# Optimization experiments

Measured on AMD Instinct MI355X. Metric: run time of the kernel, lower is better.

Reference implementation:

```python
import jax, jax.numpy as jnp
import numpy as np

B, L1, L2 = 4, 1024, 512
D_PG, D_EX = 2304, 1024
H, HKV, DH = 8, 4, 256
SCALE = 256.0 ** -0.5


def _rope(x, cos, sin):
    # x: [B, L, h, DH]; cos/sin: [B, L, 1, DH//2]
    x = x.astype(jnp.float32)
    x1, x2 = jnp.split(x, 2, axis=-1)
    return jnp.concatenate([x1 * cos - x2 * sin, x2 * cos + x1 * sin], axis=-1)


def setup_inputs() -> dict:
    key = jax.random.key(0)
    ks = jax.random.split(key, 16)
    s = 0.02
    return {
        "pg_embeds": jax.random.normal(ks[0], (B, L1, D_PG), jnp.float32),
        "ex_embeds": jax.random.normal(ks[1], (B, L2, D_EX), jnp.float32),
        "cos": jax.random.normal(ks[2], (B, L1 + L2, 1, DH // 2), jnp.float32),
        "sin": jax.random.normal(ks[3], (B, L1 + L2, 1, DH // 2), jnp.float32),
        "attention_mask": jnp.zeros((B, L1 + L2, L1 + L2), jnp.float32),
        "Wq0": jax.random.normal(ks[4], (H * DH, D_PG), jnp.float32) * s,
        "Wk0": jax.random.normal(ks[5], (HKV * DH, D_PG), jnp.float32) * s,
        "Wv0": jax.random.normal(ks[6], (HKV * DH, D_PG), jnp.float32) * s,
        "Wo0": jax.random.normal(ks[7], (D_PG, H * DH), jnp.float32) * s,
        "Wq1": jax.random.normal(ks[8], (H * DH, D_EX), jnp.float32) * s,
        "Wk1": jax.random.normal(ks[9], (HKV * DH, D_EX), jnp.float32) * s,
        "Wv1": jax.random.normal(ks[10], (HKV * DH, D_EX), jnp.float32) * s,
        "Wo1": jax.random.normal(ks[11], (D_EX, H * DH), jnp.float32) * s,
    }


def reference(pg_embeds, ex_embeds, cos, sin, attention_mask,
              Wq0, Wk0, Wv0, Wo0, Wq1, Wk1, Wv1, Wo1):
    b, l1 = pg_embeds.shape[0], pg_embeds.shape[1]
    l2 = ex_embeds.shape[1]
    # per-stream QKV projections, then concat along sequence
    q = jnp.concatenate([
        (pg_embeds @ Wq0.T).reshape(b, l1, H, DH),
        (ex_embeds @ Wq1.T).reshape(b, l2, H, DH)], axis=1)
    k = jnp.concatenate([
        (pg_embeds @ Wk0.T).reshape(b, l1, HKV, DH),
        (ex_embeds @ Wk1.T).reshape(b, l2, HKV, DH)], axis=1)
    v = jnp.concatenate([
        (pg_embeds @ Wv0.T).reshape(b, l1, HKV, DH),
        (ex_embeds @ Wv1.T).reshape(b, l2, HKV, DH)], axis=1)
    q = _rope(q, cos, sin)  # fp32
    k = _rope(k, cos, sin)
    # GQA: repeat KV heads to match query heads
    rep = H // HKV
    k = jnp.repeat(k, rep, axis=2)
    v = jnp.repeat(jnp.repeat(v, rep, axis=2).astype(jnp.float32), 1, axis=0)
    # scores: [B, H, L, L]
    scores = jnp.einsum('bqhd,bkhd->bhqk', q, k) * SCALE
    scores = scores + attention_mask[:, None, :, :]
    p = jax.nn.softmax(scores, axis=-1)
    att = jnp.einsum('bhqk,bkhd->bqhd', p, v).reshape(b, l1 + l2, H * DH)
    out0 = att[:, :l1] @ Wo0.T
    out1 = att[:, l1:] @ Wo1.T
    return (out0, out1)
```

## Files before the change

kernel.cpp:

```cpp
#include <hip/hip_runtime.h>
#include <stdint.h>
#include <stddef.h>


typedef _Float16 f16;
typedef _Float16 f16x8 __attribute__((ext_vector_type(8)));
typedef _Float16 f16x4 __attribute__((ext_vector_type(4)));
typedef float    f32x4 __attribute__((ext_vector_type(4)));

__device__ __forceinline__ void async_ld16(const void* g, void* l) {
  __builtin_amdgcn_global_load_lds((const __attribute__((address_space(1))) void*)g,
                                   (__attribute__((address_space(3))) void*)l,
                                   16, 0, 0);
}

template <typename Epi>
__device__ __forceinline__ void gemm_pipe(f16* lds,
    const f16* __restrict__ A, int lda,
    const f16* __restrict__ B, int ldb,
    int K, Epi&& epi)
{
  const int t    = threadIdx.x;
  const int w    = t >> 6;
  const int lane = t & 63;
  const int q4   = lane >> 4;
  const int l16  = lane & 15;
  const int wm   = w >> 1;
  const int wn   = w & 1;

  const int srow = w * 16 + (lane >> 2);
  const int scol = (lane & 3) * 8;
  const f16* aP = A + (size_t)srow * lda + scol;
  const f16* bP = B + (size_t)srow * ldb + scol;
  const size_t a128 = (size_t)128 * lda;
  const int wl = w * 512;

  const int arow = (wm * 64 + l16) * 32 + q4 * 8;
  const int brow = (wn * 64 + l16) * 32 + q4 * 8;

  f32x4 acc[4][4];
  const f32x4 vz = {0.f, 0.f, 0.f, 0.f};
#pragma unroll
  for (int i = 0; i < 4; ++i)
#pragma unroll
    for (int j = 0; j < 4; ++j) acc[i][j] = vz;

  async_ld16(aP,             lds + wl);
  async_ld16(aP + a128,      lds + 4096 + wl);
  async_ld16(bP,             lds + 32768 + wl);
  asm volatile("" ::: "memory");
  async_ld16(aP + 32,        lds + 8192 + wl);
  async_ld16(aP + a128 + 32, lds + 8192 + 4096 + wl);
  async_ld16(bP + 32,        lds + 32768 + 4096 + wl);
  asm volatile("s_waitcnt vmcnt(3)" ::: "memory");
  asm volatile("s_barrier" ::: "memory");

  const int NT = K >> 6;
  int cb = 0;
  for (int tk = 0; tk < NT; ++tk) {
    f16* aT = lds + cb * 16384;
    f16* bT = lds + 32768 + cb * 8192;
    f16* aD = lds + (cb ^ 1) * 16384;
    f16* bD = lds + 32768 + (cb ^ 1) * 8192;
    const int kn = (tk + 1) << 6;
    const bool st = tk < NT - 1;
#pragma unroll
    for (int s = 0; s < 2; ++s) {
      const f16* aS = aT + s * 8192;
      const f16* bS = bT + s * 4096;
      f16x8 af[4], bf[4];
#pragma unroll
      for (int i = 0; i < 4; ++i) {
        af[i] = *(const f16x8*)(aS + arow + i * 512);
        bf[i] = *(const f16x8*)(bS + brow + i * 512);
      }
      if (st) {
        if (s == 0) {
          async_ld16(aP + kn,        aD + wl);
          async_ld16(aP + a128 + kn, aD + 4096 + wl);
          async_ld16(bP + kn,        bD + wl);
        } else {
          async_ld16(aP + kn + 32,        aD + 8192 + wl);
          async_ld16(aP + a128 + kn + 32, aD + 8192 + 4096 + wl);
          async_ld16(bP + kn + 32,        bD + 4096 + wl);
        }
        asm volatile("s_waitcnt vmcnt(3)" ::: "memory");
      } else if (s == 0) {
        asm volatile("s_waitcnt vmcnt(0)" ::: "memory");
      }
      asm volatile("s_barrier" ::: "memory");
      __builtin_amdgcn_s_setprio(1);
#pragma unroll
      for (int mi = 0; mi < 4; ++mi)
#pragma unroll
        for (int ni = 0; ni < 4; ++ni)
          acc[mi][ni] = __builtin_amdgcn_mfma_f32_16x16x32_f16(af[mi], bf[ni], acc[mi][ni], 0, 0, 0);
      __builtin_amdgcn_s_setprio(0);
      asm volatile("s_barrier" ::: "memory");
    }
    cb ^= 1;
  }

#pragma unroll
  for (int mi = 0; mi < 4; ++mi)
#pragma unroll
    for (int ni = 0; ni < 4; ++ni)
#pragma unroll
      for (int r = 0; r < 4; ++r)
        epi(wm * 64 + mi * 16 + q4 * 4 + r, wn * 64 + ni * 16 + l16, acc[mi][ni][r]);
}

__global__ __launch_bounds__(512, 2) void k_qkv3(
    const f16* __restrict__ xpg, const f16* __restrict__ xex,
    const f16* __restrict__ W0,  const f16* __restrict__ W1,
    f16* __restrict__ q, f16* __restrict__ k, f16* __restrict__ v)
{
  __shared__ alignas(16) f16 lds[49152];
  const int idx = blockIdx.x;
  int by, bx, K; const f16 *A, *B;
  const bool s0 = idx < 512;
  if (s0) { by = idx >> 5; bx = idx & 31; K = 2304;
            A = xpg + (size_t)by * 256 * 2304; B = W0 + (size_t)bx * 128 * 2304; }
  else    { int j = idx - 512; by = j >> 5; bx = j & 31; K = 1024;
            A = xex + (size_t)by * 256 * 1024; B = W1 + (size_t)bx * 128 * 1024; }

  f16* D; int ldd, coff;
  if (bx < 16)      { D = q; ldd = 2048; coff = 0; }
  else if (bx < 24) { D = k; ldd = 1024; coff = 2048; }
  else              { D = v; ldd = 1024; coff = 3072; }
  const int colb = bx * 128 - coff;
  const int rowb = s0 ? ((by >> 2) * 1536 + (by & 3) * 256)
                      : ((by >> 1) * 1536 + 1024 + (by & 1) * 256);

  gemm_pipe(lds, A, K, B, K, K, [&](int r, int c, float fv) {
    D[(size_t)(rowb + r) * ldd + colb + c] = (f16)fv;
  });
}

__global__ __launch_bounds__(256) void k_post(
    f16* __restrict__ q, f16* __restrict__ k,
    const float* __restrict__ cs, const float* __restrict__ sn,
    const float* __restrict__ msk, f16* __restrict__ mkh,
    const f16* __restrict__ v, f16* __restrict__ vt)
{
  const int blk = blockIdx.x;
  if (blk < 6144) {
    __shared__ f16 tile[32][33];
    const int b = blk / 1536, r0 = blk % 1536;
    const int d0 = (r0 & 31) * 32, l0 = (r0 >> 5) * 32;
    const int t = threadIdx.x;
    const int tr = t >> 5, tc = t & 31;
#pragma unroll
    for (int i = 0; i < 4; ++i)
      tile[tr + i * 8][tc] = v[((size_t)b * 1536 + l0 + tr + i * 8) * 1024 + d0 + tc];
    __syncthreads();
#pragma unroll
    for (int i = 0; i < 4; ++i) {
      int d = d0 + tr + i * 8;
      vt[(((size_t)b * 4 + (d >> 8)) * 256 + (d & 255)) * 1536 + l0 + tc] = tile[tc][tr + i * 8];
    }
  } else if (blk < 15360) {
    const size_t gid = ((size_t)(blk - 6144) * 256 + threadIdx.x) * 4;
    float4 m4 = *(const float4*)(msk + gid);
    f16x4 o = {(f16)m4.x, (f16)m4.y, (f16)m4.z, (f16)m4.w};
    *(f16x4*)(mkh + gid) = o;
  } else {
    const size_t tid8 = ((size_t)(blk - 15360) * 256 + threadIdx.x) * 8;
    f16* base; size_t row; int col;
    if (tid8 < 12582912ull) { base = q + tid8; row = tid8 >> 11; col = (int)(tid8 & 2047); }
    else { size_t f = tid8 - 12582912ull; base = k + f; row = f >> 10; col = (int)(f & 1023); }
    const int j0 = (col & 255) >> 1;
    f16x8 x = *(const f16x8*)base;
    float4 c4 = *(const float4*)(cs + row * 128 + j0);
    float4 s4 = *(const float4*)(sn + row * 128 + j0);
    f16x8 o;
    const float cc[4] = {c4.x, c4.y, c4.z, c4.w};
    const float ss[4] = {s4.x, s4.y, s4.z, s4.w};
#pragma unroll
    for (int p = 0; p < 4; ++p) {
      float x1 = (float)x[2 * p], x2 = (float)x[2 * p + 1];
      o[2 * p]     = (f16)(x1 * cc[p] - x2 * ss[p]);
      o[2 * p + 1] = (f16)(x2 * cc[p] + x1 * ss[p]);
    }
    *(f16x8*)base = o;
  }
}

__global__ __launch_bounds__(512, 2) void k_attn2(
    const f16* __restrict__ qb, const f16* __restrict__ kb,
    const f16* __restrict__ mask, f16* __restrict__ Sdst,
    const f16* __restrict__ Psrc, const f16* __restrict__ vt,
    f16* __restrict__ att0, f16* __restrict__ att1,
    const f16* __restrict__ wo0, const f16* __restrict__ wo1,
    float* __restrict__ out0, float* __restrict__ out1,
    int b_sc, int b_pv, int b_op, int npv, int nop)
{
  __shared__ alignas(16) f16 lds[49152];
  const int idx = blockIdx.x;
  if (idx < nop) {
    int by, bx, ldc, rowb; const f16 *A, *B; float* C;
    if (idx < 72) { by = idx / 18; bx = idx % 18;
                    A = att0 + (size_t)(b_op * 4 + by) * 256 * 2048;
                    B = wo0 + (size_t)bx * 128 * 2048;
                    C = out0; ldc = 2304; rowb = b_op * 1024 + by * 256; }
    else          { int j = idx - 72; by = j >> 3; bx = j & 7;
                    A = att1 + (size_t)(b_op * 2 + by) * 256 * 2048;
                    B = wo1 + (size_t)bx * 128 * 2048;
                    C = out1; ldc = 1024; rowb = b_op * 512 + by * 256; }
    const int colb = bx * 128;
    gemm_pipe(lds, A, 2048, B, 2048, 2048, [&](int r, int c, float fv) {
      C[(size_t)(rowb + r) * ldc + colb + c] = fv;
    });
  } else if (idx < nop + npv) {
    const int j = idx - nop;
    const int h = j / 12, rem = j % 12, by = rem >> 1, bx = rem & 1;
    const f16* A = Psrc + (size_t)h * 1536 * 1536 + (size_t)by * 256 * 1536;
    const f16* B = vt + (size_t)(b_pv * 4 + (h >> 1)) * 256 * 1536 + (size_t)bx * 128 * 1536;
    f16* dst = (by < 4)
      ? att0 + (size_t)(b_pv * 1024 + by * 256) * 2048 + h * 256 + bx * 128
      : att1 + (size_t)(b_pv * 512 + (by - 4) * 256) * 2048 + h * 256 + bx * 128;
    gemm_pipe(lds, A, 1536, B, 1536, 1536, [&](int r, int c, float fv) {
      dst[(size_t)r * 2048 + c] = (f16)fv;
    });
  } else {
    const int j = idx - nop - npv;
    const int h = j / 72, rem = j % 72, by = rem / 12, bx = rem % 12;
    const f16* A = qb + (size_t)b_sc * 1536 * 2048 + h * 256 + (size_t)by * 256 * 2048;
    const f16* B = kb + (size_t)b_sc * 1536 * 1024 + (h >> 1) * 256 + (size_t)bx * 128 * 1024;
    f16* Sz = Sdst + (size_t)h * 1536 * 1536 + (size_t)by * 256 * 1536 + bx * 128;
    const f16* mb = mask + (size_t)b_sc * 1536 * 1536 + (size_t)by * 256 * 1536 + bx * 128;
    gemm_pipe(lds, A, 2048, B, 1024, 256, [&](int r, int c, float fv) {
      size_t i = (size_t)r * 1536 + c;
      Sz[i] = (f16)(fv * 0.0625f + (float)mb[i]);
    });
  }
}

__global__ __launch_bounds__(256) void k_softmax(f16* __restrict__ S)
{
  const int row = blockIdx.x * 4 + (threadIdx.x >> 6);
  const int lane = threadIdx.x & 63;
  f16* p = S + (size_t)row * 1536 + lane * 8;
  f16x8 v0 = *(const f16x8*)p;
  f16x8 v1 = *(const f16x8*)(p + 512);
  f16x8 v2 = *(const f16x8*)(p + 1024);
  float x[24];
#pragma unroll
  for (int i = 0; i < 8; ++i) {
    x[i] = (float)v0[i]; x[8 + i] = (float)v1[i]; x[16 + i] = (float)v2[i];
  }
  float mx = x[0];
#pragma unroll
  for (int i = 1; i < 24; ++i) mx = fmaxf(mx, x[i]);
#pragma unroll
  for (int o = 32; o > 0; o >>= 1) mx = fmaxf(mx, __shfl_xor(mx, o, 64));
  float s = 0.f;
#pragma unroll
  for (int i = 0; i < 24; ++i) { x[i] = __expf(x[i] - mx); s += x[i]; }
#pragma unroll
  for (int o = 32; o > 0; o >>= 1) s += __shfl_xor(s, o, 64);
  const float inv = 1.f / s;
  f16x8 o0, o1, o2;
#pragma unroll
  for (int i = 0; i < 8; ++i) {
    o0[i] = (f16)(x[i] * inv); o1[i] = (f16)(x[8 + i] * inv); o2[i] = (f16)(x[16 + i] * inv);
  }
  *(f16x8*)p = o0; *(f16x8*)(p + 512) = o1; *(f16x8*)(p + 1024) = o2;
}

__global__ __launch_bounds__(256) void k_cast_all(
    const float* __restrict__ s0, const float* __restrict__ s1,
    const float* __restrict__ s2, const float* __restrict__ s3,
    const float* __restrict__ s4, const float* __restrict__ s5,
    f16* __restrict__ ws)
{
  const size_t gid = ((size_t)blockIdx.x * 256 + threadIdx.x) * 4;
  const float* s; size_t off, dst;
  if      (gid < 9437184ull)  { s = s0; off = gid;               dst = 0ull        + off; }
  else if (gid < 11534336ull) { s = s1; off = gid - 9437184ull;  dst = 9437184ull  + off; }
  else if (gid < 13893632ull) { s = s2; off = gid - 11534336ull; dst = 18612224ull + off; }
  else if (gid < 18612224ull) { s = s3; off = gid - 13893632ull; dst = 20971520ull + off; }
  else if (gid < 19660800ull) { s = s4; off = gid - 18612224ull; dst = 28835840ull + off; }
  else                        { s = s5; off = gid - 19660800ull; dst = 29884416ull + off; }
  float4 v = *(const float4*)(s + off);
  f16x4 o = {(f16)v.x, (f16)v.y, (f16)v.z, (f16)v.w};
  *(f16x4*)(ws + dst) = o;
}

__global__ __launch_bounds__(256) void k_cast_wr(
    const float* __restrict__ wq0, const float* __restrict__ wk0,
    const float* __restrict__ wq1, const float* __restrict__ wk1,
    f16* __restrict__ W0c, f16* __restrict__ W1c)
{
  const int idx = blockIdx.x;
  const float* src; f16* dstm; int K, r, drow;
  if      (idx < 2048) { src = wq0; dstm = W0c; K = 2304; r = idx;        drow = idx; }
  else if (idx < 3072) { src = wk0; dstm = W0c; K = 2304; r = idx - 2048; drow = idx; }
  else if (idx < 5120) { src = wq1; dstm = W1c; K = 1024; r = idx - 3072; drow = idx - 3072; }
  else                 { src = wk1; dstm = W1c; K = 1024; r = idx - 5120; drow = idx - 3072; }
  const int w = r & 255;
  const int srow = (r & ~255) + (w >> 1) + ((w & 1) << 7);
  const float* sp = src + (size_t)srow * K;
  f16* dp = dstm + (size_t)drow * K;
  for (int c = threadIdx.x * 4; c < K; c += 1024) {
    float4 v = *(const float4*)(sp + c);
    f16x4 o = {(f16)v.x, (f16)v.y, (f16)v.z, (f16)v.w};
    *(f16x4*)(dp + c) = o;
  }
}

extern "C" void kernel_launch(void* const* d_in, const int* in_sizes, int n_in,
                              void* d_out, int out_size, void* d_ws, size_t ws_size,
                              hipStream_t stream)
{
  (void)in_sizes; (void)n_in; (void)out_size; (void)ws_size;
  const float* pg  = (const float*)d_in[0];
  const float* ex  = (const float*)d_in[1];
  const float* cs  = (const float*)d_in[2];
  const float* sn  = (const float*)d_in[3];
  const float* msk = (const float*)d_in[4];

  char* ws = (char*)d_ws;
  f16* xpg  = (f16*)(ws + 0);
  f16* xex  = (f16*)(ws + 18874368);
  f16* W0c  = (f16*)(ws + 23068672);
  f16* wo0c = (f16*)(ws + 41943040);
  f16* W1c  = (f16*)(ws + 51380224);
  f16* wo1c = (f16*)(ws + 59768832);
  f16* qb   = (f16*)(ws + 63963136);
  f16* kb   = (f16*)(ws + 89128960);
  f16* vb   = (f16*)(ws + 101711872);
  f16* vt   = (f16*)(ws + 114294784);
  f16* att0 = (f16*)(ws + 126877696);
  f16* att1 = (f16*)(ws + 143654912);
  f16* S0   = (f16*)(ws + 152043520);
  f16* S1   = (f16*)(ws + 189792256);
  f16* mkh  = W0c;
  float* out0 = (float*)d_out;
  float* out1 = out0 + 9437184;

  k_cast_all<<<21248, 256, 0, stream>>>(
      pg, ex, (const float*)d_in[7], (const float*)d_in[8],
      (const float*)d_in[11], (const float*)d_in[12], (f16*)ws);
  k_cast_wr<<<6144, 256, 0, stream>>>(
      (const float*)d_in[5], (const float*)d_in[6],
      (const float*)d_in[9], (const float*)d_in[10], W0c, W1c);

  k_qkv3<<<768, 512, 0, stream>>>(xpg, xex, W0c, W1c, qb, kb, vb);

  k_post<<<24576, 256, 0, stream>>>(qb, kb, cs, sn, msk, mkh, vb, vt);

  k_attn2<<<576, 512, 0, stream>>>(qb, kb, mkh, S0, S0, vt, att0, att1, wo0c, wo1c, out0, out1, 0, 0, 0, 0, 0);
  k_softmax<<<3072, 256, 0, stream>>>(S0);
  k_attn2<<<672, 512, 0, stream>>>(qb, kb, mkh, S1, S0, vt, att0, att1, wo0c, wo1c, out0, out1, 1, 0, 0, 96, 0);
  k_softmax<<<3072, 256, 0, stream>>>(S1);
  k_attn2<<<760, 512, 0, stream>>>(qb, kb, mkh, S0, S1, vt, att0, att1, wo0c, wo1c, out0, out1, 2, 1, 0, 96, 88);
  k_softmax<<<3072, 256, 0, stream>>>(S0);
  k_attn2<<<760, 512, 0, stream>>>(qb, kb, mkh, S1, S0, vt, att0, att1, wo0c, wo1c, out0, out1, 3, 2, 1, 96, 88);
  k_softmax<<<3072, 256, 0, stream>>>(S1);

  k_attn2<<<184, 512, 0, stream>>>(qb, kb, mkh, S0, S1, vt, att0, att1, wo0c, wo1c, out0, out1, 0, 3, 2, 96, 88);
  k_attn2<<<88, 512, 0, stream>>>(qb, kb, mkh, S0, S1, vt, att0, att1, wo0c, wo1c, out0, out1, 0, 0, 3, 0, 88);
}
```

Baseline: 649.2 us.

## Triple-buffer GEMM pipeline with 32-K stages, XCD block swizzle, raise occupancy bound

Replaces the double-buffered 64-wide K loop, which had two sub-steps, with a three-stage ring of 32-wide K tiles. Each stage is prefetched two iterations ahead, and there is one barrier pair per step. LDS per block shrinks from 96KB to 72KB. Blocks are remapped with an 8-way interleave so that consecutive logical tiles land on the same XCD and share L2. Launch bounds are raised to 4 blocks per CU. Asking for that occupancy may force register caps that spill the 64-float accumulator, and the LDS footprint may still only allow 2 blocks per CU.

```diff
diff --git a/kernel.cpp b/kernel.cpp
--- a/kernel.cpp
+++ b/kernel.cpp
@@ -12,6 +12,10 @@
   __builtin_amdgcn_global_load_lds((const __attribute__((address_space(1))) void*)g,
                                    (__attribute__((address_space(3))) void*)l,
                                    16, 0, 0);
+}
+
+__device__ __forceinline__ int xswz(int bid, int n) {
+  return (bid & 7) * (n >> 3) + (bid >> 3);
 }
 
 template <typename Epi>
@@ -45,61 +49,46 @@
 #pragma unroll
     for (int j = 0; j < 4; ++j) acc[i][j] = vz;
 
-  async_ld16(aP,             lds + wl);
-  async_ld16(aP + a128,      lds + 4096 + wl);
-  async_ld16(bP,             lds + 32768 + wl);
+#define STAGE3(kt, bi)                                            \
+  { const int kk_ = (kt) << 5; f16* d_ = lds + (bi) * 12288;      \
+    async_ld16(aP + kk_,        d_ + wl);                         \
+    async_ld16(aP + a128 + kk_, d_ + 4096 + wl);                  \
+    async_ld16(bP + kk_,        d_ + 8192 + wl); }
+
+  STAGE3(0, 0);
   asm volatile("" ::: "memory");
-  async_ld16(aP + 32,        lds + 8192 + wl);
-  async_ld16(aP + a128 + 32, lds + 8192 + 4096 + wl);
-  async_ld16(bP + 32,        lds + 32768 + 4096 + wl);
-  asm volatile("s_waitcnt vmcnt(3)" ::: "memory");
-  asm volatile("s_barrier" ::: "memory");
-
-  const int NT = K >> 6;
-  int cb = 0;
+  STAGE3(1, 1);
+
+  const int NT = K >> 5;
+  int cur = 0;
   for (int tk = 0; tk < NT; ++tk) {
-    f16* aT = lds + cb * 16384;
-    f16* bT = lds + 32768 + cb * 8192;
-    f16* aD = lds + (cb ^ 1) * 16384;
-    f16* bD = lds + 32768 + (cb ^ 1) * 8192;
-    const int kn = (tk + 1) << 6;
-    const bool st = tk < NT - 1;
-#pragma unroll
-    for (int s = 0; s < 2; ++s) {
-      const f16* aS = aT + s * 8192;
-      const f16* bS = bT + s * 4096;
-      f16x8 af[4], bf[4];
-#pragma unroll
-      for (int i = 0; i < 4; ++i) {
-        af[i] = *(const f16x8*)(aS + arow + i * 512);
-        bf[i] = *(const f16x8*)(bS + brow + i * 512);
-      }
-      if (st) {
-        if (s == 0) {
-          async_ld16(aP + kn,        aD + wl);
-          async_ld16(aP + a128 + kn, aD + 4096 + wl);
-          async_ld16(bP + kn,        bD + wl);
-        } else {
-          async_ld16(aP + kn + 32,        aD + 8192 + wl);
-          async_ld16(aP + a128 + kn + 32, aD + 8192 + 4096 + wl);
-          async_ld16(bP + kn + 32,        bD + 4096 + wl);
-        }
-        asm volatile("s_waitcnt vmcnt(3)" ::: "memory");
-      } else if (s == 0) {
-        asm volatile("s_waitcnt vmcnt(0)" ::: "memory");
-      }
-      asm volatile("s_barrier" ::: "memory");
-      __builtin_amdgcn_s_setprio(1);
-#pragma unroll
-      for (int mi = 0; mi < 4; ++mi)
-#pragma unroll
-        for (int ni = 0; ni < 4; ++ni)
-          acc[mi][ni] = __builtin_amdgcn_mfma_f32_16x16x32_f16(af[mi], bf[ni], acc[mi][ni], 0, 0, 0);
-      __builtin_amdgcn_s_setprio(0);
-      asm volatile("s_barrier" ::: "memory");
+    if (tk == NT - 1) asm volatile("s_waitcnt vmcnt(0)" ::: "memory");
+    else              asm volatile("s_waitcnt vmcnt(3)" ::: "memory");
+    asm volatile("s_barrier" ::: "memory");
+
+    const f16* aS = lds + cur * 12288;
+    const f16* bS = aS + 8192;
+    f16x8 af[4], bf[4];
+#pragma unroll
+    for (int i = 0; i < 4; ++i) {
+      af[i] = *(const f16x8*)(aS + arow + i * 512);
+      bf[i] = *(const f16x8*)(bS + brow + i * 512);
     }
-    cb ^= 1;
-  }
+    if (tk + 2 < NT) {
+      int nb = cur + 2; if (nb >= 3) nb -= 3;
+      STAGE3(tk + 2, nb);
+    }
+    __builtin_amdgcn_s_setprio(1);
+#pragma unroll
+    for (int mi = 0; mi < 4; ++mi)
+#pragma unroll
+      for (int ni = 0; ni < 4; ++ni)
+        acc[mi][ni] = __builtin_amdgcn_mfma_f32_16x16x32_f16(af[mi], bf[ni], acc[mi][ni], 0, 0, 0);
+    __builtin_amdgcn_s_setprio(0);
+    asm volatile("s_barrier" ::: "memory");
+    ++cur; if (cur == 3) cur = 0;
+  }
+#undef STAGE3
 
 #pragma unroll
   for (int mi = 0; mi < 4; ++mi)
@@ -110,13 +99,13 @@
         epi(wm * 64 + mi * 16 + q4 * 4 + r, wn * 64 + ni * 16 + l16, acc[mi][ni][r]);
 }
 
-__global__ __launch_bounds__(512, 2) void k_qkv3(
+__global__ __launch_bounds__(512, 4) void k_qkv4(
     const f16* __restrict__ xpg, const f16* __restrict__ xex,
     const f16* __restrict__ W0,  const f16* __restrict__ W1,
     f16* __restrict__ q, f16* __restrict__ k, f16* __restrict__ v)
 {
-  __shared__ alignas(16) f16 lds[49152];
-  const int idx = blockIdx.x;
+  __shared__ alignas(16) f16 lds[36864];
+  const int idx = xswz(blockIdx.x, 768);
   int by, bx, K; const f16 *A, *B;
   const bool s0 = idx < 512;
   if (s0) { by = idx >> 5; bx = idx & 31; K = 2304;
@@ -186,7 +175,7 @@
   }
 }
 
-__global__ __launch_bounds__(512, 2) void k_attn2(
+__global__ __launch_bounds__(512, 4) void k_attn3(
     const f16* __restrict__ qb, const f16* __restrict__ kb,
     const f16* __restrict__ mask, f16* __restrict__ Sdst,
     const f16* __restrict__ Psrc, const f16* __restrict__ vt,
@@ -195,8 +184,8 @@
     float* __restrict__ out0, float* __restrict__ out1,
     int b_sc, int b_pv, int b_op, int npv, int nop)
 {
-  __shared__ alignas(16) f16 lds[49152];
-  const int idx = blockIdx.x;
+  __shared__ alignas(16) f16 lds[36864];
+  const int idx = xswz(blockIdx.x, (int)gridDim.x);
   if (idx < nop) {
     int by, bx, ldc, rowb; const f16 *A, *B; float* C;
     if (idx < 72) { by = idx / 18; bx = idx % 18;
@@ -346,19 +335,19 @@
       (const float*)d_in[5], (const float*)d_in[6],
       (const float*)d_in[9], (const float*)d_in[10], W0c, W1c);
 
-  k_qkv3<<<768, 512, 0, stream>>>(xpg, xex, W0c, W1c, qb, kb, vb);
+  k_qkv4<<<768, 512, 0, stream>>>(xpg, xex, W0c, W1c, qb, kb, vb);
 
   k_post<<<24576, 256, 0, stream>>>(qb, kb, cs, sn, msk, mkh, vb, vt);
 
-  k_attn2<<<576, 512, 0, stream>>>(qb, kb, mkh, S0, S0, vt, att0, att1, wo0c, wo1c, out0, out1, 0, 0, 0, 0, 0);
+  k_attn3<<<576, 512, 0, stream>>>(qb, kb, mkh, S0, S0, vt, att0, att1, wo0c, wo1c, out0, out1, 0, 0, 0, 0, 0);
   k_softmax<<<3072, 256, 0, stream>>>(S0);
-  k_attn2<<<672, 512, 0, stream>>>(qb, kb, mkh, S1, S0, vt, att0, att1, wo0c, wo1c, out0, out1, 1, 0, 0, 96, 0);
+  k_attn3<<<672, 512, 0, stream>>>(qb, kb, mkh, S1, S0, vt, att0, att1, wo0c, wo1c, out0, out1, 1, 0, 0, 96, 0);
   k_softmax<<<3072, 256, 0, stream>>>(S1);
-  k_attn2<<<760, 512, 0, stream>>>(qb, kb, mkh, S0, S1, vt, att0, att1, wo0c, wo1c, out0, out1, 2, 1, 0, 96, 88);
+  k_attn3<<<760, 512, 0, stream>>>(qb, kb, mkh, S0, S1, vt, att0, att1, wo0c, wo1c, out0, out1, 2, 1, 0, 96, 88);
   k_softmax<<<3072, 256, 0, stream>>>(S0);
-  k_attn2<<<760, 512, 0, stream>>>(qb, kb, mkh, S1, S0, vt, att0, att1, wo0c, wo1c, out0, out1, 3, 2, 1, 96, 88);
+  k_attn3<<<760, 512, 0, stream>>>(qb, kb, mkh, S1, S0, vt, att0, att1, wo0c, wo1c, out0, out1, 3, 2, 1, 96, 88);
   k_softmax<<<3072, 256, 0, stream>>>(S1);
 
-  k_attn2<<<184, 512, 0, stream>>>(qb, kb, mkh, S0, S1, vt, att0, att1, wo0c, wo1c, out0, out1, 0, 3, 2, 96, 88);
-  k_attn2<<<88, 512, 0, stream>>>(qb, kb, mkh, S0, S1, vt, att0, att1, wo0c, wo1c, out0, out1, 0, 0, 3, 0, 88);
-}
+  k_attn3<<<184, 512, 0, stream>>>(qb, kb, mkh, S0, S1, vt, att0, att1, wo0c, wo1c, out0, out1, 0, 3, 2, 96, 88);
+  k_attn3<<<88, 512, 0, stream>>>(qb, kb, mkh, S0, S1, vt, att0, att1, wo0c, wo1c, out0, out1, 0, 0, 3, 0, 88);
+}
```

Result: slower. 757.1 us (+16.6%).

## Use 256x256 output tiles for the fused QKV projection GEMM

Applied to the files above, without the earlier changes.

Adds a new GEMM routine in which each 512-thread block computes a 256x256 tile: 8 waves in a 2x4 layout, each holding 8x4 MFMA accumulators, with double-buffered async global-to-LDS loads over 64-wide K steps. The QKV kernel now launches 384 blocks instead of 768 and uses 128KB of LDS. Larger tiles raise arithmetic intensity and cut redundant A/B loads. In exchange, register pressure goes up (128 accumulator floats per thread) and there are fewer blocks across the CUs, which could hurt occupancy and load balance.

```diff
diff --git a/kernel.cpp b/kernel.cpp
--- a/kernel.cpp
+++ b/kernel.cpp
@@ -12,6 +12,95 @@
   __builtin_amdgcn_global_load_lds((const __attribute__((address_space(1))) void*)g,
                                    (__attribute__((address_space(3))) void*)l,
                                    16, 0, 0);
+}
+
+template <typename Epi>
+__device__ __forceinline__ void gemm256(f16* lds,
+    const f16* __restrict__ A, int lda,
+    const f16* __restrict__ B, int ldb,
+    int K, Epi&& epi)
+{
+  const int t    = threadIdx.x;
+  const int w    = t >> 6;
+  const int lane = t & 63;
+  const int q4   = lane >> 4;
+  const int l16  = lane & 15;
+  const int wm   = w >> 2;
+  const int wn   = w & 3;
+
+  f16* ldsA = lds;
+  f16* ldsB = lds + 32768;
+
+  const f16* aP = A + (size_t)(lane >> 2) * lda + (lane & 3) * 8;
+  const f16* bP = B + (size_t)(lane >> 2) * ldb + (lane & 3) * 8;
+  const size_t aR0 = (size_t)(w * 32) * lda;
+  const size_t aR1 = aR0 + (size_t)16 * lda;
+  const size_t bR0 = (size_t)(w * 32) * ldb;
+  const size_t bR1 = bR0 + (size_t)16 * ldb;
+  const int wo = w * 1024;
+
+  const int arow = (wm * 128 + l16) * 32 + q4 * 8;
+  const int brow = (wn * 64 + l16) * 32 + q4 * 8;
+
+  f32x4 acc[8][4];
+  const f32x4 vz = {0.f, 0.f, 0.f, 0.f};
+#pragma unroll
+  for (int i = 0; i < 8; ++i)
+#pragma unroll
+    for (int j = 0; j < 4; ++j) acc[i][j] = vz;
+
+#pragma unroll
+  for (int s = 0; s < 2; ++s) {
+    const int kk = s * 32;
+    async_ld16(aP + aR0 + kk, ldsA + s * 8192 + wo);
+    async_ld16(aP + aR1 + kk, ldsA + s * 8192 + wo + 512);
+    async_ld16(bP + bR0 + kk, ldsB + s * 8192 + wo);
+    async_ld16(bP + bR1 + kk, ldsB + s * 8192 + wo + 512);
+  }
+
+  const int NT = K >> 6;
+  for (int tk = 0; tk < NT; ++tk) {
+    const int d  = (tk & 1) ? 16384 : 0;
+    const int dn = 16384 - d;
+    const bool st = tk + 1 < NT;
+    const int kn = (tk + 1) << 6;
+#pragma unroll
+    for (int s = 0; s < 2; ++s) {
+      if (s == 0 || st) asm volatile("s_waitcnt vmcnt(4)" ::: "memory");
+      else              asm volatile("s_waitcnt vmcnt(0)" ::: "memory");
+      asm volatile("s_barrier" ::: "memory");
+      const f16* aS = ldsA + d + s * 8192;
+      const f16* bS = ldsB + d + s * 8192;
+      f16x8 af[8], bf[4];
+#pragma unroll
+      for (int i = 0; i < 8; ++i) af[i] = *(const f16x8*)(aS + arow + i * 512);
+#pragma unroll
+      for (int i = 0; i < 4; ++i) bf[i] = *(const f16x8*)(bS + brow + i * 512);
+      if (st) {
+        const int kk = kn + s * 32;
+        async_ld16(aP + aR0 + kk, ldsA + dn + s * 8192 + wo);
+        async_ld16(aP + aR1 + kk, ldsA + dn + s * 8192 + wo + 512);
+        async_ld16(bP + bR0 + kk, ldsB + dn + s * 8192 + wo);
+        async_ld16(bP + bR1 + kk, ldsB + dn + s * 8192 + wo + 512);
+      }
+      __builtin_amdgcn_s_setprio(1);
+#pragma unroll
+      for (int mi = 0; mi < 8; ++mi)
+#pragma unroll
+        for (int ni = 0; ni < 4; ++ni)
+          acc[mi][ni] = __builtin_amdgcn_mfma_f32_16x16x32_f16(af[mi], bf[ni], acc[mi][ni], 0, 0, 0);
+      __builtin_amdgcn_s_setprio(0);
+      asm volatile("s_barrier" ::: "memory");
+    }
+  }
+
+#pragma unroll
+  for (int mi = 0; mi < 8; ++mi)
+#pragma unroll
+    for (int ni = 0; ni < 4; ++ni)
+#pragma unroll
+      for (int r = 0; r < 4; ++r)
+        epi(wm * 128 + mi * 16 + q4 * 4 + r, wn * 64 + ni * 16 + l16, acc[mi][ni][r]);
 }
 
 template <typename Epi>
@@ -110,29 +199,29 @@
         epi(wm * 64 + mi * 16 + q4 * 4 + r, wn * 64 + ni * 16 + l16, acc[mi][ni][r]);
 }
 
-__global__ __launch_bounds__(512, 2) void k_qkv3(
+__global__ __launch_bounds__(512, 2) void k_qkv5(
     const f16* __restrict__ xpg, const f16* __restrict__ xex,
     const f16* __restrict__ W0,  const f16* __restrict__ W1,
     f16* __restrict__ q, f16* __restrict__ k, f16* __restrict__ v)
 {
-  __shared__ alignas(16) f16 lds[49152];
+  __shared__ alignas(16) f16 lds[65536];
   const int idx = blockIdx.x;
   int by, bx, K; const f16 *A, *B;
-  const bool s0 = idx < 512;
-  if (s0) { by = idx >> 5; bx = idx & 31; K = 2304;
-            A = xpg + (size_t)by * 256 * 2304; B = W0 + (size_t)bx * 128 * 2304; }
-  else    { int j = idx - 512; by = j >> 5; bx = j & 31; K = 1024;
-            A = xex + (size_t)by * 256 * 1024; B = W1 + (size_t)bx * 128 * 1024; }
+  const bool s0 = idx < 256;
+  if (s0) { by = idx >> 4; bx = idx & 15; K = 2304;
+            A = xpg + (size_t)by * 256 * 2304; B = W0 + (size_t)bx * 256 * 2304; }
+  else    { int j = idx - 256; by = j >> 4; bx = j & 15; K = 1024;
+            A = xex + (size_t)by * 256 * 1024; B = W1 + (size_t)bx * 256 * 1024; }
 
   f16* D; int ldd, coff;
-  if (bx < 16)      { D = q; ldd = 2048; coff = 0; }
-  else if (bx < 24) { D = k; ldd = 1024; coff = 2048; }
+  if (bx < 8)       { D = q; ldd = 2048; coff = 0; }
+  else if (bx < 12) { D = k; ldd = 1024; coff = 2048; }
   else              { D = v; ldd = 1024; coff = 3072; }
-  const int colb = bx * 128 - coff;
+  const int colb = bx * 256 - coff;
   const int rowb = s0 ? ((by >> 2) * 1536 + (by & 3) * 256)
                       : ((by >> 1) * 1536 + 1024 + (by & 1) * 256);
 
-  gemm_pipe(lds, A, K, B, K, K, [&](int r, int c, float fv) {
+  gemm256(lds, A, K, B, K, K, [&](int r, int c, float fv) {
     D[(size_t)(rowb + r) * ldd + colb + c] = (f16)fv;
   });
 }
@@ -346,7 +435,7 @@
       (const float*)d_in[5], (const float*)d_in[6],
       (const float*)d_in[9], (const float*)d_in[10], W0c, W1c);
 
-  k_qkv3<<<768, 512, 0, stream>>>(xpg, xex, W0c, W1c, qb, kb, vb);
+  k_qkv5<<<384, 512, 0, stream>>>(xpg, xex, W0c, W1c, qb, kb, vb);
 
   k_post<<<24576, 256, 0, stream>>>(qb, kb, cs, sn, msk, mkh, vb, vt);
 
```

After: 642.8 us. No clear change (-1.0%).
